# Optimization experiments

Hardware: AMD Instinct MI355X
Metric: run time of the kernel (lower is better)

Reference implementation:

```python
import jax, jax.numpy as jnp
import numpy as np

B = 131072
IN = 128
H = 128

def setup_inputs() -> dict:
    key = jax.random.key(0)
    ks = jax.random.split(key, 12)
    # kaiming-normal-ish init for weights (std ~ sqrt(2/fan_out))
    std_w = (2.0 / H) ** 0.5
    inp = {
        'x': jax.random.normal(ks[0], (B, IN), dtype=jnp.float32),
        'h_prev': jax.random.normal(ks[1], (B, H), dtype=jnp.float32),
        'c_prev': jax.random.normal(ks[2], (B, H), dtype=jnp.float32),
        'Wi': jax.random.normal(ks[3], (IN, H), dtype=jnp.float32) * std_w,
        'Ui': jax.random.normal(ks[4], (H, H), dtype=jnp.float32) * std_w,
        'bi': jnp.ones((H,), dtype=jnp.float32),
        'Wf': jax.random.normal(ks[5], (IN, H), dtype=jnp.float32) * std_w,
        'Uf': jax.random.normal(ks[6], (H, H), dtype=jnp.float32) * std_w,
        'bf': jnp.ones((H,), dtype=jnp.float32),
        'Wg': jax.random.normal(ks[7], (IN, H), dtype=jnp.float32) * std_w,
        'Ug': jax.random.normal(ks[8], (H, H), dtype=jnp.float32) * std_w,
        'bg': jnp.ones((H,), dtype=jnp.float32),
        'Wo': jax.random.normal(ks[9], (IN, H), dtype=jnp.float32) * std_w,
        'Uo': jax.random.normal(ks[10], (H, H), dtype=jnp.float32) * std_w,
        'bo': jnp.ones((H,), dtype=jnp.float32),
    }
    return inp

def reference(x, h_prev, c_prev, Wi, Ui, bi, Wf, Uf, bf, Wg, Ug, bg, Wo, Uo, bo):
    # Faithful per-gate math (i, f, o sigmoid gates; g tanh candidate)
    ig = jax.nn.sigmoid(x @ Wi + h_prev @ Ui + bi)
    fg = jax.nn.sigmoid(x @ Wf + h_prev @ Uf + bf)
    og = jax.nn.sigmoid(x @ Wo + h_prev @ Uo + bo)
    cc = jnp.tanh(x @ Wg + h_prev @ Ug + bg)
    c = fg * c_prev + ig * cc
    h = og * jnp.tanh(c)
    return (h, c)
```

## Files before the change

### kernel.cpp

```cpp
#include <hip/hip_runtime.h>


#define B_ROWS 131072
#define HDIM 128
#define KDIM 256
#define BM 32
#define LDA 264

typedef __attribute__((ext_vector_type(4))) float f32x4;
typedef __attribute__((ext_vector_type(8))) short s16x8;

__device__ inline unsigned short f2bf(float f) {
    unsigned int u = __float_as_uint(f);
    u += 0x7fffu + ((u >> 16) & 1u);
    return (unsigned short)(u >> 16);
}

__device__ inline float frcp(float x) { return __builtin_amdgcn_rcpf(x); }
__device__ inline float fsigmoid(float x) { return frcp(1.0f + __expf(-x)); }
__device__ inline float ftanh(float x) { return 1.0f - 2.0f * frcp(__expf(2.0f * x) + 1.0f); }

__global__ void prep_weights(const float* __restrict__ Wi, const float* __restrict__ Ui,
                             const float* __restrict__ Wf, const float* __restrict__ Uf,
                             const float* __restrict__ Wg, const float* __restrict__ Ug,
                             const float* __restrict__ Wo, const float* __restrict__ Uo,
                             unsigned short* __restrict__ Bp) {
    int idx = blockIdx.x * 256 + threadIdx.x;
    int c = idx >> 8;
    int k = idx & 255;
    int w = c >> 6;
    int gate = (c >> 4) & 3;
    int t = c & 15;
    int j = w * 16 + t;
    const float* Wp = gate == 0 ? Wi : gate == 1 ? Wf : gate == 2 ? Wg : Wo;
    const float* Up = gate == 0 ? Ui : gate == 1 ? Uf : gate == 2 ? Ug : Uo;
    float v = (k < 128) ? Wp[k * HDIM + j] : Up[(k - 128) * HDIM + j];
    Bp[idx] = f2bf(v);
}

__global__ __launch_bounds__(512, 4) void lstm_main(
    const float* __restrict__ x, const float* __restrict__ h_prev,
    const float* __restrict__ c_prev,
    const unsigned short* __restrict__ Bp,
    const float* __restrict__ bi, const float* __restrict__ bf_,
    const float* __restrict__ bg, const float* __restrict__ bo,
    float* __restrict__ out)
{
    __shared__ unsigned short At[BM * LDA];

    const int tid = threadIdx.x;
    const int m0 = blockIdx.x * BM;

    #pragma unroll
    for (int it = 0; it < 4; ++it) {
        int fi = tid + it * 512;
        int r = fi >> 6;
        int c4 = fi & 63;
        const float* src = (c4 < 32) ? (x + (size_t)(m0 + r) * HDIM + c4 * 4)
                                     : (h_prev + (size_t)(m0 + r) * HDIM + (c4 - 32) * 4);
        float4 v = *(const float4*)src;
        ushort4 p;
        p.x = f2bf(v.x); p.y = f2bf(v.y); p.z = f2bf(v.z); p.w = f2bf(v.w);
        *(ushort4*)&At[r * LDA + c4 * 4] = p;
    }
    __syncthreads();

    const int wave = tid >> 6;
    const int lane = tid & 63;
    const int t16 = lane & 15;
    const int q = lane >> 4;

    f32x4 acc[2][4];
    const f32x4 zero = {0.0f, 0.0f, 0.0f, 0.0f};
    #pragma unroll
    for (int mi = 0; mi < 2; ++mi)
        #pragma unroll
        for (int ni = 0; ni < 4; ++ni)
            acc[mi][ni] = zero;

    const unsigned short* bbase = Bp + (size_t)(wave * 64 + t16) * KDIM + q * 8;

    #pragma unroll
    for (int kc = 0; kc < 8; ++kc) {
        const int k = kc * 32 + q * 8;
        s16x8 a[2], b[4];
        #pragma unroll
        for (int mi = 0; mi < 2; ++mi)
            a[mi] = *(const s16x8*)&At[(mi * 16 + t16) * LDA + k];
        #pragma unroll
        for (int ni = 0; ni < 4; ++ni)
            b[ni] = *(const s16x8*)(bbase + ni * 16 * KDIM + kc * 32);
        #pragma unroll
        for (int mi = 0; mi < 2; ++mi)
            #pragma unroll
            for (int ni = 0; ni < 4; ++ni)
                acc[mi][ni] = __builtin_amdgcn_mfma_f32_16x16x32_bf16(a[mi], b[ni], acc[mi][ni], 0, 0, 0);
    }

    const int j = wave * 16 + t16;
    const float vbi = bi[j], vbf = bf_[j], vbg = bg[j], vbo = bo[j];
    float* hout = out;
    float* cout = out + (size_t)B_ROWS * HDIM;

    #pragma unroll
    for (int mi = 0; mi < 2; ++mi) {
        #pragma unroll
        for (int r = 0; r < 4; ++r) {
            int row = m0 + mi * 16 + q * 4 + r;
            size_t off = (size_t)row * HDIM + j;
            float cp = c_prev[off];
            float ig = fsigmoid(acc[mi][0][r] + vbi);
            float fg = fsigmoid(acc[mi][1][r] + vbf);
            float cc = ftanh(acc[mi][2][r] + vbg);
            float og = fsigmoid(acc[mi][3][r] + vbo);
            float c = fg * cp + ig * cc;
            float h = og * ftanh(c);
            hout[off] = h;
            cout[off] = c;
        }
    }
}

extern "C" void kernel_launch(void* const* d_in, const int* in_sizes, int n_in,
                              void* d_out, int out_size, void* d_ws, size_t ws_size,
                              hipStream_t stream) {
    const float* x      = (const float*)d_in[0];
    const float* h_prev = (const float*)d_in[1];
    const float* c_prev = (const float*)d_in[2];
    const float* Wi = (const float*)d_in[3];
    const float* Ui = (const float*)d_in[4];
    const float* bi = (const float*)d_in[5];
    const float* Wf = (const float*)d_in[6];
    const float* Uf = (const float*)d_in[7];
    const float* bf = (const float*)d_in[8];
    const float* Wg = (const float*)d_in[9];
    const float* Ug = (const float*)d_in[10];
    const float* bg = (const float*)d_in[11];
    const float* Wo = (const float*)d_in[12];
    const float* Uo = (const float*)d_in[13];
    const float* bo = (const float*)d_in[14];

    unsigned short* Bp = (unsigned short*)d_ws;

    prep_weights<<<512, 256, 0, stream>>>(Wi, Ui, Wf, Uf, Wg, Ug, Wo, Uo, Bp);
    lstm_main<<<B_ROWS / BM, 512, 0, stream>>>(x, h_prev, c_prev, Bp, bi, bf, bg, bo, (float*)d_out);
}
```

Before: 376.8 us.

## Double row tile to 64 and pre-swizzle A/B into MFMA fragment order

```diff
diff --git a/kernel.cpp b/kernel.cpp
--- a/kernel.cpp
+++ b/kernel.cpp
@@ -4,8 +4,7 @@
 #define B_ROWS 131072
 #define HDIM 128
 #define KDIM 256
-#define BM 32
-#define LDA 264
+#define BM 64
 
 typedef __attribute__((ext_vector_type(4))) float f32x4;
 typedef __attribute__((ext_vector_type(8))) short s16x8;
@@ -26,14 +25,16 @@
                              const float* __restrict__ Wo, const float* __restrict__ Uo,
                              unsigned short* __restrict__ Bp) {
     int idx = blockIdx.x * 256 + threadIdx.x;
-    int c = idx >> 8;
-    int k = idx & 255;
-    int w = c >> 6;
-    int gate = (c >> 4) & 3;
-    int t = c & 15;
-    int j = w * 16 + t;
-    const float* Wp = gate == 0 ? Wi : gate == 1 ? Wf : gate == 2 ? Wg : Wo;
-    const float* Up = gate == 0 ? Ui : gate == 1 ? Uf : gate == 2 ? Ug : Uo;
+    int e   = idx & 7;
+    int q   = (idx >> 3) & 3;
+    int t16 = (idx >> 5) & 15;
+    int ni  = (idx >> 9) & 3;
+    int kc  = (idx >> 11) & 7;
+    int w   = idx >> 14;
+    int j = w * 16 + t16;
+    int k = kc * 32 + q * 8 + e;
+    const float* Wp = ni == 0 ? Wi : ni == 1 ? Wf : ni == 2 ? Wg : Wo;
+    const float* Up = ni == 0 ? Ui : ni == 1 ? Uf : ni == 2 ? Ug : Uo;
     float v = (k < 128) ? Wp[k * HDIM + j] : Up[(k - 128) * HDIM + j];
     Bp[idx] = f2bf(v);
 }
@@ -46,22 +47,25 @@
     const float* __restrict__ bg, const float* __restrict__ bo,
     float* __restrict__ out)
 {
-    __shared__ unsigned short At[BM * LDA];
+    __shared__ unsigned short As[4 * 8 * 512];
 
     const int tid = threadIdx.x;
     const int m0 = blockIdx.x * BM;
 
     #pragma unroll
-    for (int it = 0; it < 4; ++it) {
-        int fi = tid + it * 512;
-        int r = fi >> 6;
+    for (int it = 0; it < 8; ++it) {
+        int fi = it * 512 + tid;
+        int r  = fi >> 6;
         int c4 = fi & 63;
-        const float* src = (c4 < 32) ? (x + (size_t)(m0 + r) * HDIM + c4 * 4)
-                                     : (h_prev + (size_t)(m0 + r) * HDIM + (c4 - 32) * 4);
+        int k0 = c4 * 4;
+        const float* src = (k0 < 128) ? (x + (size_t)(m0 + r) * HDIM + k0)
+                                      : (h_prev + (size_t)(m0 + r) * HDIM + (k0 - 128));
         float4 v = *(const float4*)src;
         ushort4 p;
         p.x = f2bf(v.x); p.y = f2bf(v.y); p.z = f2bf(v.z); p.w = f2bf(v.w);
-        *(ushort4*)&At[r * LDA + c4 * 4] = p;
+        int mi = r >> 4, t16r = r & 15;
+        int kc = k0 >> 5, qq = (k0 >> 3) & 3, e0 = k0 & 7;
+        *(ushort4*)&As[((mi * 8 + kc) * 16 + t16r) * 32 + qq * 8 + e0] = p;
     }
     __syncthreads();
 
@@ -69,29 +73,29 @@
     const int lane = tid & 63;
     const int t16 = lane & 15;
     const int q = lane >> 4;
+    const int lane_off = t16 * 32 + q * 8;
 
-    f32x4 acc[2][4];
+    f32x4 acc[4][4];
     const f32x4 zero = {0.0f, 0.0f, 0.0f, 0.0f};
     #pragma unroll
-    for (int mi = 0; mi < 2; ++mi)
+    for (int mi = 0; mi < 4; ++mi)
         #pragma unroll
         for (int ni = 0; ni < 4; ++ni)
             acc[mi][ni] = zero;
 
-    const unsigned short* bbase = Bp + (size_t)(wave * 64 + t16) * KDIM + q * 8;
+    const unsigned short* bbase = Bp + (size_t)(wave * 8) * 2048 + lane_off;
 
     #pragma unroll
     for (int kc = 0; kc < 8; ++kc) {
-        const int k = kc * 32 + q * 8;
-        s16x8 a[2], b[4];
-        #pragma unroll
-        for (int mi = 0; mi < 2; ++mi)
-            a[mi] = *(const s16x8*)&At[(mi * 16 + t16) * LDA + k];
+        s16x8 a[4], b[4];
         #pragma unroll
         for (int ni = 0; ni < 4; ++ni)
-            b[ni] = *(const s16x8*)(bbase + ni * 16 * KDIM + kc * 32);
+            b[ni] = *(const s16x8*)(bbase + kc * 2048 + ni * 512);
         #pragma unroll
-        for (int mi = 0; mi < 2; ++mi)
+        for (int mi = 0; mi < 4; ++mi)
+            a[mi] = *(const s16x8*)&As[(mi * 8 + kc) * 512 + lane_off];
+        #pragma unroll
+        for (int mi = 0; mi < 4; ++mi)
             #pragma unroll
             for (int ni = 0; ni < 4; ++ni)
                 acc[mi][ni] = __builtin_amdgcn_mfma_f32_16x16x32_bf16(a[mi], b[ni], acc[mi][ni], 0, 0, 0);
@@ -102,18 +106,24 @@
     float* hout = out;
     float* cout = out + (size_t)B_ROWS * HDIM;
 
+    float cp[4][4];
     #pragma unroll
-    for (int mi = 0; mi < 2; ++mi) {
+    for (int mi = 0; mi < 4; ++mi)
+        #pragma unroll
+        for (int r = 0; r < 4; ++r)
+            cp[mi][r] = c_prev[(size_t)(m0 + mi * 16 + q * 4 + r) * HDIM + j];
+
+    #pragma unroll
+    for (int mi = 0; mi < 4; ++mi) {
         #pragma unroll
         for (int r = 0; r < 4; ++r) {
             int row = m0 + mi * 16 + q * 4 + r;
             size_t off = (size_t)row * HDIM + j;
-            float cp = c_prev[off];
             float ig = fsigmoid(acc[mi][0][r] + vbi);
             float fg = fsigmoid(acc[mi][1][r] + vbf);
             float cc = ftanh(acc[mi][2][r] + vbg);
             float og = fsigmoid(acc[mi][3][r] + vbo);
-            float c = fg * cp + ig * cc;
+            float c = fg * cp[mi][r] + ig * cc;
             float h = og * ftanh(c);
             hout[off] = h;
             cout[off] = c;
```

Result: faster. 347.7 us (-7.7%).
